# Optimization experiments

Measured on AMD Instinct MI355X. Metric: run time of the kernel, lower is better.

## Reference

```python
import jax, jax.numpy as jnp
import numpy as np

C = 256        # channels
H = 8          # num_heads
DH = C // H    # head dim
WIN = 512      # window size
STRIDE = 256
HID = 512      # ffn hidden = 2.0 * C
LENGTHS = [6400, 6400, 6400, 6400]
N = sum(LENGTHS)
EPS = 1e-5


def _build_windows(lengths, W, stride):
    # mirrors build_windows_1d: overlapping windows per segment, padded + masked
    idxs, masks = [], []
    start = 0
    for L in lengths:
        n_windows = max(0, L - 1) // stride + 1
        for i in range(n_windows):
            s = i * stride
            b = min(L, s + W)
            l = b - s
            loc = np.arange(s, b, dtype=np.int32) + start
            if l < W:
                loc = np.concatenate([loc, np.full(W - l, loc[-1], dtype=np.int32)])
            m = np.zeros(W, dtype=bool)
            m[:l] = True
            idxs.append(loc)
            masks.append(m)
        start += L
    return np.stack(idxs, 0), np.stack(masks, 0)


def _layernorm(x, w, b):
    mu = jnp.mean(x, axis=-1, keepdims=True)
    var = jnp.mean(jnp.square(x - mu), axis=-1, keepdims=True)
    return (x - mu) * jax.lax.rsqrt(var + EPS) * w + b


def setup_inputs() -> dict:
    key = jax.random.key(0)
    ks = jax.random.split(key, 8)
    win_idx_np, win_mask_np = _build_windows(LENGTHS, WIN, STRIDE)
    p = lambda k, shape: jax.random.normal(k, shape, dtype=jnp.float32) * 0.02
    return {
        "x": jax.random.normal(ks[0], (N, C), dtype=jnp.float32),
        "win_idx": jnp.asarray(win_idx_np, dtype=jnp.int32),
        "win_mask": jnp.asarray(win_mask_np),
        "ln1_w": jnp.ones((C,), jnp.float32),
        "ln1_b": jnp.zeros((C,), jnp.float32),
        "w_qkv": p(ks[1], (3 * C, C)),
        "w_proj": p(ks[2], (C, C)),
        "b_proj": jnp.zeros((C,), jnp.float32),
        "ln2_w": jnp.ones((C,), jnp.float32),
        "ln2_b": jnp.zeros((C,), jnp.float32),
        "w1": p(ks[3], (HID, C)),
        "b1": jnp.zeros((HID,), jnp.float32),
        "bn_w": jnp.ones((HID,), jnp.float32),
        "bn_b": jnp.zeros((HID,), jnp.float32),
        "w2": p(ks[4], (C, HID)),
        "b2": jnp.zeros((C,), jnp.float32),
    }


def reference(x, win_idx, win_mask, ln1_w, ln1_b, w_qkv, w_proj, b_proj,
              ln2_w, ln2_b, w1, b1, bn_w, bn_b, w2, b2):
    M, W = win_idx.shape
    x_in = _layernorm(x, ln1_w, ln1_b)                      # [N, C]
    g = x_in[win_idx]                                        # [M, W, C] gather
    qkv = (g @ w_qkv.T).reshape(M, W, 3, H, DH)
    qkv = jnp.moveaxis(qkv, (2, 3), (0, 2))                  # [3, M, H, W, DH]
    q, k, v = qkv[0], qkv[1], qkv[2]
    scores = jnp.einsum("mhqd,mhkd->mhqk", q, k) / jnp.sqrt(jnp.asarray(DH, x.dtype))
    scores = jnp.where(win_mask[:, None, None, :], scores, -jnp.inf)
    attn = jax.nn.softmax(scores, axis=-1)                   # [M, H, W, W]
    out = jnp.einsum("mhqk,mhkd->mhqd", attn, v)            # [M, H, W, DH]
    out = jnp.moveaxis(out, 1, 2).reshape(M, W, C)
    out_proj = (out @ w_proj.T + b_proj) * win_mask[..., None]
    flat_idx = win_idx.reshape(-1)
    y = jnp.zeros_like(x).at[flat_idx].add(out_proj.reshape(-1, C))
    counts = jnp.zeros((x.shape[0], 1), x.dtype).at[flat_idx].add(
        win_mask.reshape(-1, 1).astype(x.dtype))
    x1 = x + y / jnp.maximum(counts, 1.0)
    # FFN with training-mode BatchNorm1d (default norm_layer)
    h = _layernorm(x1, ln2_w, ln2_b) @ w1.T + b1             # [N, HID]
    mu = jnp.mean(h, axis=0)
    var = jnp.mean(jnp.square(h - mu), axis=0)
    h = (h - mu) * jax.lax.rsqrt(var + EPS) * bn_w + bn_b
    h = jax.nn.relu(h)
    return x1 + (h @ w2.T + b2)
```

## Files before the change

### kernel.cpp

```cpp
#include <hip/hip_runtime.h>

#define C_DIM 256
#define HID_DIM 512
#define NHEAD 8
#define DHEAD 32
#define WWIN 512

typedef __attribute__((ext_vector_type(8))) short frag_ab;
typedef __attribute__((ext_vector_type(4))) short frag4;
typedef __attribute__((ext_vector_type(4))) float f32x4;

__device__ __forceinline__ float bf2f(unsigned int u16) {
    return __uint_as_float(u16 << 16);
}
__device__ __forceinline__ unsigned short f2bf(float f) {
    unsigned int x = __float_as_uint(f);
    return (unsigned short)((x + 0x7fffu + ((x >> 16) & 1u)) >> 16);
}
__device__ __forceinline__ void unpack8(uint4 u, float* d) {
    d[0] = bf2f(u.x & 0xffffu); d[1] = bf2f(u.x >> 16);
    d[2] = bf2f(u.y & 0xffffu); d[3] = bf2f(u.y >> 16);
    d[4] = bf2f(u.z & 0xffffu); d[5] = bf2f(u.z >> 16);
    d[6] = bf2f(u.w & 0xffffu); d[7] = bf2f(u.w >> 16);
}
__device__ __forceinline__ unsigned int pk2(float lo, float hi) {
    return __builtin_amdgcn_perm(__float_as_uint(hi), __float_as_uint(lo), 0x07060302u);
}
__device__ __forceinline__ void async_cp16(const void* g, void* l) {
    __builtin_amdgcn_global_load_lds(
        (const __attribute__((address_space(1))) unsigned int*)g,
        (__attribute__((address_space(3))) unsigned int*)l, 16, 0, 0);
}

__global__ __launch_bounds__(256) void rowstats_k(const float* __restrict__ X,
        float* __restrict__ mu, float* __restrict__ rs) {
    int lane = threadIdx.x & 63;
    int row = blockIdx.x * 4 + (threadIdx.x >> 6);
    float4 v = ((const float4*)(X + (size_t)row * C_DIM))[lane];
    float s = v.x + v.y + v.z + v.w;
    float q = v.x * v.x + v.y * v.y + v.z * v.z + v.w * v.w;
    #pragma unroll
    for (int o = 32; o; o >>= 1) { s += __shfl_xor(s, o); q += __shfl_xor(q, o); }
    if (lane == 0) {
        float m = s * (1.0f / C_DIM);
        float var = q * (1.0f / C_DIM) - m * m;
        mu[row] = m; rs[row] = rsqrtf(var + 1e-5f);
    }
}

__global__ __launch_bounds__(512) void wininv_k(const int* __restrict__ widx,
        int* __restrict__ wlen, int* __restrict__ cnt, int* __restrict__ inv) {
    int m = blockIdx.x, j = threadIdx.x;
    int id = widx[m * WWIN + j];
    int valid = (j == 0) || (id != widx[m * WWIN + j - 1]);
    __shared__ int part[8];
    int v = valid;
    #pragma unroll
    for (int o = 32; o; o >>= 1) v += __shfl_xor(v, o);
    if ((j & 63) == 0) part[j >> 6] = v;
    __syncthreads();
    if (j == 0) {
        int s = 0;
        #pragma unroll
        for (int i = 0; i < 8; i++) s += part[i];
        wlen[m] = s;
    }
    if (valid) {
        int slot = atomicAdd(&cnt[id], 1);
        if (slot < 2) inv[id * 2 + slot] = m * WWIN + j;
    }
}

__global__ __launch_bounds__(256) void cvtw_k(
        const float* __restrict__ a, const float* __restrict__ b,
        const float* __restrict__ c, const float* __restrict__ d,
        unsigned short* __restrict__ oa, unsigned short* __restrict__ ob,
        unsigned short* __restrict__ oc, unsigned short* __restrict__ od) {
    int bi = blockIdx.x;
    const float* src; unsigned short* dst; int base;
    if (bi < 192)      { src = a; dst = oa; base = bi; }
    else if (bi < 256) { src = b; dst = ob; base = bi - 192; }
    else if (bi < 384) { src = c; dst = oc; base = bi - 256; }
    else               { src = d; dst = od; base = bi - 384; }
    int i = base * 1024 + threadIdx.x * 4;
    float4 v = *(const float4*)(src + i);
    ushort4 o;
    o.x = f2bf(v.x); o.y = f2bf(v.y); o.z = f2bf(v.z); o.w = f2bf(v.w);
    *(ushort4*)(dst + i) = o;
}

template<int K, int AMODE, int OMODE>
__global__ __launch_bounds__(256, 3) void mgemm_k(
        const void* __restrict__ Av, const unsigned short* __restrict__ Bw,
        const float* __restrict__ bias, void* __restrict__ Outv,
        const float* __restrict__ rowmu, const float* __restrict__ rowrs,
        const float* __restrict__ colw, const float* __restrict__ colb,
        const float* __restrict__ resid, float* __restrict__ hsum,
        float* __restrict__ hsq, int CN, int AM) {
    __shared__ unsigned short As[4096];
    __shared__ unsigned short Bs[4096];
    const int t = threadIdx.x;
    const int w = t >> 6, lane = t & 63;
    const int Q = lane >> 4, n = lane & 15;
    const int r0 = blockIdx.y * 128, c0 = blockIdx.x * 128;
    const int qr0 = (w & 1) * 64, qc0 = (w >> 1) * 64;
    const f32x4 z4 = {0.f, 0.f, 0.f, 0.f};
    f32x4 acc[4][4];
    #pragma unroll
    for (int i = 0; i < 4; i++)
        #pragma unroll
        for (int j = 0; j < 4; j++) acc[i][j] = z4;

    for (int k0 = 0; k0 < K; k0 += 32) {
        if (k0) __syncthreads();
        #pragma unroll
        for (int i = 0; i < 2; i++) {
            int sbase = w * 128 + i * 64;
            int l = sbase + lane;
            int col = l >> 2;
            int sub = ((l & 3) - (col >> 1)) & 3;
            async_cp16(Bw + (size_t)(c0 + col) * K + k0 + sub * 8, &Bs[sbase * 8]);
        }
        if constexpr (AMODE == 0 || AMODE == 4) {
            #pragma unroll
            for (int i = 0; i < 2; i++) {
                int sbase = w * 128 + i * 64;
                int l = sbase + lane;
                int row = l >> 2;
                int sub = ((l & 3) - (row >> 1)) & 3;
                const unsigned short* src;
                if constexpr (AMODE == 0)
                    src = (const unsigned short*)Av + (size_t)(r0 + row) * K + k0 + sub * 8;
                else
                    src = (const unsigned short*)Av + (size_t)k0 * AM + (size_t)(r0 + row) * 32 + sub * 8;
                async_cp16(src, &As[sbase * 8]);
            }
        } else {
            #pragma unroll
            for (int ii = 0; ii < 2; ii++) {
                int s = t + ii * 256;
                int row = s >> 2;
                int sub = ((s & 3) - (row >> 1)) & 3;
                const float* src = (const float*)Av + (size_t)(r0 + row) * K + k0 + sub * 8;
                float4 v0 = ((const float4*)src)[0];
                float4 v1 = ((const float4*)src)[1];
                float f[8] = {v0.x, v0.y, v0.z, v0.w, v1.x, v1.y, v1.z, v1.w};
                float4 cw0 = *(const float4*)(colw + k0 + sub * 8);
                float4 cw1 = *(const float4*)(colw + k0 + sub * 8 + 4);
                float4 cb0 = *(const float4*)(colb + k0 + sub * 8);
                float4 cb1 = *(const float4*)(colb + k0 + sub * 8 + 4);
                float cw[8] = {cw0.x, cw0.y, cw0.z, cw0.w, cw1.x, cw1.y, cw1.z, cw1.w};
                float cb[8] = {cb0.x, cb0.y, cb0.z, cb0.w, cb1.x, cb1.y, cb1.z, cb1.w};
                if constexpr (AMODE == 1) {
                    float rm = rowmu[r0 + row], rv = rowrs[r0 + row];
                    #pragma unroll
                    for (int j = 0; j < 8; j++) f[j] = (f[j] - rm) * rv * cw[j] + cb[j];
                } else {
                    #pragma unroll
                    for (int j = 0; j < 8; j++) f[j] = fmaxf(f[j] * cw[j] + cb[j], 0.f);
                }
                uint4 pkd;
                pkd.x = pk2(f[0], f[1]); pkd.y = pk2(f[2], f[3]);
                pkd.z = pk2(f[4], f[5]); pkd.w = pk2(f[6], f[7]);
                *(uint4*)&As[s * 8] = pkd;
            }
        }
        asm volatile("s_waitcnt vmcnt(0)" ::: "memory");
        __syncthreads();
        const int asub = (Q + (n >> 1)) & 3;
        frag_ab af[4], bfr[4];
        #pragma unroll
        for (int i = 0; i < 4; i++) {
            af[i]  = *(const frag_ab*)&As[((qr0 + i * 16 + n) * 4 + asub) * 8];
            bfr[i] = *(const frag_ab*)&Bs[((qc0 + i * 16 + n) * 4 + asub) * 8];
        }
        #pragma unroll
        for (int rt = 0; rt < 4; rt++)
            #pragma unroll
            for (int ct = 0; ct < 4; ct++)
                acc[rt][ct] = __builtin_amdgcn_mfma_f32_16x16x32_bf16(
                    af[rt], bfr[ct], acc[rt][ct], 0, 0, 0);
    }

    if constexpr (OMODE == 5) {
        __shared__ unsigned short Ts[4][16 * 72];
        unsigned short* tb = Ts[w];
        #pragma unroll
        for (int rt = 0; rt < 4; rt++) {
            #pragma unroll
            for (int ct = 0; ct < 4; ct++) {
                f32x4 a = acc[rt][ct];
                #pragma unroll
                for (int i = 0; i < 4; i++)
                    tb[(Q * 4 + i) * 72 + ct * 16 + n] = f2bf(a[i]);
            }
            int r2 = lane >> 2, sg = lane & 3;
            uint4 v0 = *(const uint4*)&tb[r2 * 72 + sg * 16];
            uint4 v1 = *(const uint4*)&tb[r2 * 72 + sg * 16 + 8];
            int mrow = r0 + qr0 + rt * 16 + r2;
            int ccb = c0 + qc0 + sg * 16;
            int plane = ((ccb >> 8) << 3) | ((ccb >> 5) & 7);
            unsigned short* dst = (unsigned short*)Outv +
                ((size_t)plane * CN + mrow) * 32 + (ccb & 31);
            *(uint4*)dst = v0;
            *(uint4*)(dst + 8) = v1;
        }
        return;
    }
    float sc[4] = {0.f, 0.f, 0.f, 0.f}, qc[4] = {0.f, 0.f, 0.f, 0.f};
    #pragma unroll
    for (int rt = 0; rt < 4; rt++) {
        #pragma unroll
        for (int ct = 0; ct < 4; ct++) {
            int mrow = r0 + qr0 + rt * 16 + Q * 4;
            int ccol = c0 + qc0 + ct * 16 + n;
            f32x4 a = acc[rt][ct];
            if constexpr (OMODE == 0) {
                unsigned short* dst = (unsigned short*)Outv + (size_t)mrow * CN + ccol;
                #pragma unroll
                for (int i = 0; i < 4; i++) dst[(size_t)i * CN] = f2bf(a[i]);
            } else if constexpr (OMODE == 1) {
                float bb = bias[ccol];
                unsigned short* dst = (unsigned short*)Outv + (size_t)mrow * CN + ccol;
                #pragma unroll
                for (int i = 0; i < 4; i++) dst[(size_t)i * CN] = f2bf(a[i] + bb);
            } else if constexpr (OMODE == 2) {
                float bb = bias[ccol];
                float* dst = (float*)Outv + (size_t)mrow * CN + ccol;
                #pragma unroll
                for (int i = 0; i < 4; i++) dst[(size_t)i * CN] = a[i] + bb;
            } else if constexpr (OMODE == 3) {
                float bb = bias[ccol];
                float* dst = (float*)Outv + (size_t)mrow * CN + ccol;
                #pragma unroll
                for (int i = 0; i < 4; i++) {
                    float v = a[i] + bb;
                    dst[(size_t)i * CN] = v;
                    sc[ct] += v; qc[ct] += v * v;
                }
            } else {
                float bb = bias[ccol];
                float* dst = (float*)Outv + (size_t)mrow * CN + ccol;
                const float* rr = resid + (size_t)mrow * CN + ccol;
                #pragma unroll
                for (int i = 0; i < 4; i++) dst[(size_t)i * CN] = a[i] + bb + rr[(size_t)i * CN];
            }
        }
    }
    if constexpr (OMODE == 3) {
        #pragma unroll
        for (int ct = 0; ct < 4; ct++) {
            float s = sc[ct], q2 = qc[ct];
            s += __shfl_xor(s, 16); s += __shfl_xor(s, 32);
            q2 += __shfl_xor(q2, 16); q2 += __shfl_xor(q2, 32);
            if (Q == 0) {
                int ccol = c0 + qc0 + ct * 16 + n;
                atomicAdd(&hsum[ccol], s);
                atomicAdd(&hsq[ccol], q2);
            }
        }
    }
}

#define KSTR 40
#define VSTR 136
#define TSTR 40
__global__ __launch_bounds__(256, 4) void attn_mfma_k(
        const unsigned short* __restrict__ qkv, const int* __restrict__ widx,
        const int* __restrict__ wlen, unsigned short* __restrict__ aout,
        int N, int MW) {
    __shared__ unsigned short Kl[128 * KSTR];
    __shared__ unsigned short Vt[32 * VSTR];
    __shared__ unsigned short Ts[4][16 * TSTR];
    const int mh = blockIdx.x >> 1, half = blockIdx.x & 1;
    const int m = mh >> 3, h = mh & 7;
    const int len = wlen[m];
    if (half && len <= 256) return;
    const int t = threadIdx.x;
    const int w = t >> 6, lane = t & 63;
    const int Q = lane >> 4, n = lane & 15;
    const int qbase = half * 256 + w * 64;
    const int* wrow = widx + m * WWIN;
    const unsigned short* Qp = qkv + (size_t)h * N * 32;
    const unsigned short* Kp = qkv + (size_t)(8 + h) * N * 32;
    const unsigned short* Vp = qkv + (size_t)(16 + h) * N * 32;
    const f32x4 z4 = {0.f, 0.f, 0.f, 0.f};

    const float qs = 0.17677669529663687f * 1.4426950408889634f;
    frag_ab qf[4];
    #pragma unroll
    for (int qt = 0; qt < 4; qt++) {
        int tok = wrow[qbase + qt * 16 + n];
        uint4 u = *(const uint4*)(Qp + (size_t)tok * 32 + Q * 8);
        float f[8]; unpack8(u, f);
        uint4 r;
        r.x = pk2(f[0] * qs, f[1] * qs); r.y = pk2(f[2] * qs, f[3] * qs);
        r.z = pk2(f[4] * qs, f[5] * qs); r.w = pk2(f[6] * qs, f[7] * qs);
        qf[qt] = __builtin_bit_cast(frag_ab, r);
    }

    f32x4 Ot[2][4];
    #pragma unroll
    for (int dt = 0; dt < 2; dt++)
        #pragma unroll
        for (int qt = 0; qt < 4; qt++) Ot[dt][qt] = z4;
    float rsum[4] = {0.f, 0.f, 0.f, 0.f};

    const int nchunk = (len + 127) >> 7;
    for (int c = 0; c < nchunk; c++) {
        const int kb = c << 7;
        __syncthreads();
        if (t < 128) {
            int r = t;
            int tok = wrow[kb + r];
            const uint4* src = (const uint4*)(Vp + (size_t)tok * 32);
            #pragma unroll
            for (int i = 0; i < 4; i++) {
                uint4 u = src[i];
                unsigned short* vp = &Vt[(i * 8) * VSTR + r];
                vp[0 * VSTR] = (unsigned short)(u.x & 0xffffu);
                vp[1 * VSTR] = (unsigned short)(u.x >> 16);
                vp[2 * VSTR] = (unsigned short)(u.y & 0xffffu);
                vp[3 * VSTR] = (unsigned short)(u.y >> 16);
                vp[4 * VSTR] = (unsigned short)(u.z & 0xffffu);
                vp[5 * VSTR] = (unsigned short)(u.z >> 16);
                vp[6 * VSTR] = (unsigned short)(u.w & 0xffffu);
                vp[7 * VSTR] = (unsigned short)(u.w >> 16);
            }
        } else {
            int r = t - 128;
            int tok = wrow[kb + r];
            const uint4* src = (const uint4*)(Kp + (size_t)tok * 32);
            #pragma unroll
            for (int i = 0; i < 4; i++) {
                int c4 = (r + i) & 3;
                *(uint4*)&Kl[r * KSTR + c4 * 8] = src[c4];
            }
        }
        __syncthreads();
        int rem = len - kb; if (rem > 128) rem = 128;
        const int nsub = (rem + 31) >> 5;
        for (int s = 0; s < nsub; s++) {
            const int lim = rem - s * 32;
            frag_ab kf0 = *(const frag_ab*)&Kl[(s * 32 + n) * KSTR + Q * 8];
            frag_ab kf1 = *(const frag_ab*)&Kl[(s * 32 + 16 + n) * KSTR + Q * 8];
            frag4 va00 = *(const frag4*)&Vt[n * VSTR + s * 32 + 4 * Q];
            frag4 va01 = *(const frag4*)&Vt[n * VSTR + s * 32 + 16 + 4 * Q];
            frag4 va10 = *(const frag4*)&Vt[(16 + n) * VSTR + s * 32 + 4 * Q];
            frag4 va11 = *(const frag4*)&Vt[(16 + n) * VSTR + s * 32 + 16 + 4 * Q];
            #pragma unroll
            for (int qt = 0; qt < 4; qt++) {
                f32x4 s0 = __builtin_amdgcn_mfma_f32_16x16x32_bf16(kf0, qf[qt], z4, 0, 0, 0);
                f32x4 s1 = __builtin_amdgcn_mfma_f32_16x16x32_bf16(kf1, qf[qt], z4, 0, 0, 0);
                float e[8];
                #pragma unroll
                for (int i = 0; i < 4; i++) {
                    e[i]     = __builtin_amdgcn_exp2f(s0[i]);
                    e[4 + i] = __builtin_amdgcn_exp2f(s1[i]);
                }
                if (lim < 32) {
                    #pragma unroll
                    for (int i = 0; i < 4; i++) {
                        if (4 * Q + i >= lim)      e[i] = 0.f;
                        if (16 + 4 * Q + i >= lim) e[4 + i] = 0.f;
                    }
                }
                float rsq = rsum[qt];
                #pragma unroll
                for (int i = 0; i < 8; i++) rsq += e[i];
                rsum[qt] = rsq;
                uint2 u0, u1;
                u0.x = pk2(e[0], e[1]); u0.y = pk2(e[2], e[3]);
                u1.x = pk2(e[4], e[5]); u1.y = pk2(e[6], e[7]);
                frag4 p0 = __builtin_bit_cast(frag4, u0);
                frag4 p1 = __builtin_bit_cast(frag4, u1);
                Ot[0][qt] = __builtin_amdgcn_mfma_f32_16x16x16bf16_1k(va00, p0, Ot[0][qt], 0, 0, 0);
                Ot[0][qt] = __builtin_amdgcn_mfma_f32_16x16x16bf16_1k(va01, p1, Ot[0][qt], 0, 0, 0);
                Ot[1][qt] = __builtin_amdgcn_mfma_f32_16x16x16bf16_1k(va10, p0, Ot[1][qt], 0, 0, 0);
                Ot[1][qt] = __builtin_amdgcn_mfma_f32_16x16x16bf16_1k(va11, p1, Ot[1][qt], 0, 0, 0);
            }
        }
    }

    unsigned short* tb = Ts[w];
    const int r2 = lane >> 2, sg = lane & 3;
    #pragma unroll
    for (int qt = 0; qt < 4; qt++) {
        float r = rsum[qt];
        r += __shfl_xor(r, 16);
        r += __shfl_xor(r, 32);
        float inv = 1.f / r;
        #pragma unroll
        for (int dt = 0; dt < 2; dt++) {
            f32x4 o = Ot[dt][qt];
            uint2 pk;
            pk.x = pk2(o[0] * inv, o[1] * inv);
            pk.y = pk2(o[2] * inv, o[3] * inv);
            *(uint2*)&tb[n * TSTR + dt * 16 + 4 * Q] = pk;
        }
        uint4 v = *(const uint4*)&tb[r2 * TSTR + sg * 8];
        unsigned short* dst = aout +
            ((size_t)h * MW + (size_t)(m * WWIN + qbase + qt * 16 + r2)) * 32 + sg * 8;
        *(uint4*)dst = v;
    }
}

__global__ __launch_bounds__(256) void combine_k(
        const float* __restrict__ x, const unsigned short* __restrict__ proj,
        const int* __restrict__ cnt, const int* __restrict__ inv,
        float* __restrict__ x1, float* __restrict__ mu, float* __restrict__ rs) {
    int lane = threadIdx.x & 63;
    int row = blockIdx.x * 4 + (threadIdx.x >> 6);
    int c = cnt[row];
    if (c > 2) c = 2;
    float4 acc = make_float4(0.f, 0.f, 0.f, 0.f);
    for (int s = 0; s < c; s++) {
        int src = inv[row * 2 + s];
        uint2 p = ((const uint2*)(proj + (size_t)src * C_DIM))[lane];
        acc.x += bf2f(p.x & 0xffffu); acc.y += bf2f(p.x >> 16);
        acc.z += bf2f(p.y & 0xffffu); acc.w += bf2f(p.y >> 16);
    }
    float ic = 1.f / (float)(c > 0 ? c : 1);
    float4 xv = ((const float4*)(x + (size_t)row * C_DIM))[lane];
    float4 r4;
    r4.x = xv.x + acc.x * ic; r4.y = xv.y + acc.y * ic;
    r4.z = xv.z + acc.z * ic; r4.w = xv.w + acc.w * ic;
    ((float4*)(x1 + (size_t)row * C_DIM))[lane] = r4;
    float s = r4.x + r4.y + r4.z + r4.w;
    float q = r4.x * r4.x + r4.y * r4.y + r4.z * r4.z + r4.w * r4.w;
    #pragma unroll
    for (int o = 32; o; o >>= 1) { s += __shfl_xor(s, o); q += __shfl_xor(q, o); }
    if (lane == 0) {
        float mm = s * (1.f / C_DIM);
        float var = q * (1.f / C_DIM) - mm * mm;
        mu[row] = mm; rs[row] = rsqrtf(var + 1e-5f);
    }
}

__global__ void bnfin_k(const float* __restrict__ hsum, const float* __restrict__ hsq,
        const float* __restrict__ bnw, const float* __restrict__ bnb,
        float* __restrict__ premul, float* __restrict__ preadd, float inv_n) {
    int c = threadIdx.x;
    float m = hsum[c] * inv_n;
    float var = hsq[c] * inv_n - m * m;
    float rstd = rsqrtf(var + 1e-5f);
    float pm = rstd * bnw[c];
    premul[c] = pm;
    preadd[c] = bnb[c] - m * pm;
}

extern "C" void kernel_launch(void* const* d_in, const int* in_sizes, int n_in,
                              void* d_out, int out_size, void* d_ws, size_t ws_size,
                              hipStream_t stream) {
    const float* x    = (const float*)d_in[0];
    const int* widx   = (const int*)d_in[1];
    const float* ln1w = (const float*)d_in[3];
    const float* ln1b = (const float*)d_in[4];
    const float* wqkv = (const float*)d_in[5];
    const float* wproj = (const float*)d_in[6];
    const float* bproj = (const float*)d_in[7];
    const float* ln2w = (const float*)d_in[8];
    const float* ln2b = (const float*)d_in[9];
    const float* w1   = (const float*)d_in[10];
    const float* b1   = (const float*)d_in[11];
    const float* bnw  = (const float*)d_in[12];
    const float* bnb  = (const float*)d_in[13];
    const float* w2   = (const float*)d_in[14];
    const float* b2   = (const float*)d_in[15];
    float* out = (float*)d_out;

    const int N  = in_sizes[0] / C_DIM;
    const int MW = in_sizes[1];
    const int M  = MW / WWIN;

    char* w = (char*)d_ws;
    size_t off = 0;
    auto alloc = [&](size_t bytes) -> void* {
        void* p = w + off;
        off += (bytes + 255) & ~(size_t)255;
        return p;
    };
    size_t szA = (size_t)MW * C_DIM * 4;
    void* regA = alloc(szA);
    unsigned short* qkv = (unsigned short*)regA;
    unsigned short* out_proj = (unsigned short*)regA;
    float* hbuf = (float*)regA;
    size_t szB = (size_t)MW * C_DIM * 2;
    void* regB = alloc(szB);
    unsigned short* attn_out = (unsigned short*)regB;
    float* x1 = (float*)regB;

    unsigned short* wqkv_bf = (unsigned short*)alloc(768 * 256 * 2);
    unsigned short* wproj_bf = (unsigned short*)alloc(256 * 256 * 2);
    unsigned short* w1_bf = (unsigned short*)alloc(512 * 256 * 2);
    unsigned short* w2_bf = (unsigned short*)alloc(256 * 512 * 2);

    float* mu0 = (float*)alloc((size_t)N * 4);
    float* rs0 = (float*)alloc((size_t)N * 4);
    float* mu1 = (float*)alloc((size_t)N * 4);
    float* rs1 = (float*)alloc((size_t)N * 4);
    int* cnt   = (int*)alloc((size_t)N * 4);
    int* inv   = (int*)alloc((size_t)N * 8);
    int* wlen  = (int*)alloc((size_t)M * 4);
    float* hsum = (float*)alloc(HID_DIM * 4);
    float* hsq  = (float*)alloc(HID_DIM * 4);
    float* premul = (float*)alloc(HID_DIM * 4);
    float* preadd = (float*)alloc(HID_DIM * 4);

    hipMemsetAsync(cnt, 0, (size_t)N * 4, stream);
    hipMemsetAsync(hsum, 0, HID_DIM * 4, stream);
    hipMemsetAsync(hsq, 0, HID_DIM * 4, stream);

    cvtw_k<<<512, 256, 0, stream>>>(wqkv, wproj, w1, w2, wqkv_bf, wproj_bf, w1_bf, w2_bf);
    rowstats_k<<<N / 4, 256, 0, stream>>>(x, mu0, rs0);
    wininv_k<<<M, 512, 0, stream>>>(widx, wlen, cnt, inv);
    mgemm_k<256, 1, 5><<<dim3(768 / 128, N / 128), 256, 0, stream>>>(
        x, wqkv_bf, nullptr, qkv, mu0, rs0, ln1w, ln1b, nullptr, nullptr, nullptr, N, 0);
    attn_mfma_k<<<M * NHEAD * 2, 256, 0, stream>>>(qkv, widx, wlen, attn_out, N, MW);
    mgemm_k<256, 4, 1><<<dim3(256 / 128, MW / 128), 256, 0, stream>>>(
        attn_out, wproj_bf, bproj, out_proj, nullptr, nullptr, nullptr, nullptr,
        nullptr, nullptr, nullptr, 256, MW);
    combine_k<<<N / 4, 256, 0, stream>>>(x, out_proj, cnt, inv, x1, mu1, rs1);
    mgemm_k<256, 1, 3><<<dim3(512 / 128, N / 128), 256, 0, stream>>>(
        x1, w1_bf, b1, hbuf, mu1, rs1, ln2w, ln2b, nullptr, hsum, hsq, 512, 0);
    bnfin_k<<<1, HID_DIM, 0, stream>>>(hsum, hsq, bnw, bnb, premul, preadd, 1.0f / (float)N);
    mgemm_k<512, 3, 4><<<dim3(256 / 128, N / 128), 256, 0, stream>>>(
        hbuf, w2_bf, b2, out, nullptr, nullptr, premul, preadd, x1, nullptr, nullptr, 256, 0);
}
```

Before: 300.3 us.

## Precompute LayerNorm outputs as bf16 and store GEMM intermediates in bf16

LayerNorm1 and LayerNorm2 are now applied in the row-stats and combine kernels, which write normalized bf16 activations. The QKV and FFN1 GEMMs can then load A tiles with async global-to-LDS copies instead of fp32 loads plus in-register normalization. The FFN hidden buffer and out_proj now go through an LDS-transposed bf16 epilogue with coalesced 16-byte stores, and the FFN2 A loader reads bf16 rather than fp32. This trades extra bf16 activation writes and reads for halved intermediate traffic and simpler GEMM prologues, at some precision cost because BN statistics are taken before bf16 rounding.

```diff
diff --git a/kernel.cpp b/kernel.cpp
--- a/kernel.cpp
+++ b/kernel.cpp
@@ -32,8 +32,9 @@
         (__attribute__((address_space(3))) unsigned int*)l, 16, 0, 0);
 }
 
-__global__ __launch_bounds__(256) void rowstats_k(const float* __restrict__ X,
-        float* __restrict__ mu, float* __restrict__ rs) {
+__global__ __launch_bounds__(256) void ln1_k(const float* __restrict__ X,
+        const float* __restrict__ wv, const float* __restrict__ bv,
+        unsigned short* __restrict__ out) {
     int lane = threadIdx.x & 63;
     int row = blockIdx.x * 4 + (threadIdx.x >> 6);
     float4 v = ((const float4*)(X + (size_t)row * C_DIM))[lane];
@@ -41,11 +42,14 @@
     float q = v.x * v.x + v.y * v.y + v.z * v.z + v.w * v.w;
     #pragma unroll
     for (int o = 32; o; o >>= 1) { s += __shfl_xor(s, o); q += __shfl_xor(q, o); }
-    if (lane == 0) {
-        float m = s * (1.0f / C_DIM);
-        float var = q * (1.0f / C_DIM) - m * m;
-        mu[row] = m; rs[row] = rsqrtf(var + 1e-5f);
-    }
+    float mm = s * (1.f / C_DIM);
+    float rv = rsqrtf(q * (1.f / C_DIM) - mm * mm + 1e-5f);
+    float4 w4 = ((const float4*)wv)[lane];
+    float4 b4 = ((const float4*)bv)[lane];
+    uint2 o2;
+    o2.x = pk2((v.x - mm) * rv * w4.x + b4.x, (v.y - mm) * rv * w4.y + b4.y);
+    o2.y = pk2((v.z - mm) * rv * w4.z + b4.z, (v.w - mm) * rv * w4.w + b4.w);
+    ((uint2*)(out + (size_t)row * C_DIM))[lane] = o2;
 }
 
 __global__ __launch_bounds__(512) void wininv_k(const int* __restrict__ widx,
@@ -93,7 +97,6 @@
 __global__ __launch_bounds__(256, 3) void mgemm_k(
         const void* __restrict__ Av, const unsigned short* __restrict__ Bw,
         const float* __restrict__ bias, void* __restrict__ Outv,
-        const float* __restrict__ rowmu, const float* __restrict__ rowrs,
         const float* __restrict__ colw, const float* __restrict__ colb,
         const float* __restrict__ resid, float* __restrict__ hsum,
         float* __restrict__ hsq, int CN, int AM) {
@@ -141,24 +144,17 @@
                 int s = t + ii * 256;
                 int row = s >> 2;
                 int sub = ((s & 3) - (row >> 1)) & 3;
-                const float* src = (const float*)Av + (size_t)(r0 + row) * K + k0 + sub * 8;
-                float4 v0 = ((const float4*)src)[0];
-                float4 v1 = ((const float4*)src)[1];
-                float f[8] = {v0.x, v0.y, v0.z, v0.w, v1.x, v1.y, v1.z, v1.w};
+                uint4 u = *(const uint4*)((const unsigned short*)Av +
+                        (size_t)(r0 + row) * K + k0 + sub * 8);
+                float f[8]; unpack8(u, f);
                 float4 cw0 = *(const float4*)(colw + k0 + sub * 8);
                 float4 cw1 = *(const float4*)(colw + k0 + sub * 8 + 4);
                 float4 cb0 = *(const float4*)(colb + k0 + sub * 8);
                 float4 cb1 = *(const float4*)(colb + k0 + sub * 8 + 4);
                 float cw[8] = {cw0.x, cw0.y, cw0.z, cw0.w, cw1.x, cw1.y, cw1.z, cw1.w};
                 float cb[8] = {cb0.x, cb0.y, cb0.z, cb0.w, cb1.x, cb1.y, cb1.z, cb1.w};
-                if constexpr (AMODE == 1) {
-                    float rm = rowmu[r0 + row], rv = rowrs[r0 + row];
-                    #pragma unroll
-                    for (int j = 0; j < 8; j++) f[j] = (f[j] - rm) * rv * cw[j] + cb[j];
-                } else {
-                    #pragma unroll
-                    for (int j = 0; j < 8; j++) f[j] = fmaxf(f[j] * cw[j] + cb[j], 0.f);
-                }
+                #pragma unroll
+                for (int j = 0; j < 8; j++) f[j] = fmaxf(f[j] * cw[j] + cb[j], 0.f);
                 uint4 pkd;
                 pkd.x = pk2(f[0], f[1]); pkd.y = pk2(f[2], f[3]);
                 pkd.z = pk2(f[4], f[5]); pkd.w = pk2(f[6], f[7]);
@@ -182,32 +178,57 @@
                     af[rt], bfr[ct], acc[rt][ct], 0, 0, 0);
     }
 
-    if constexpr (OMODE == 5) {
+    if constexpr (OMODE == 5 || OMODE == 6 || OMODE == 7) {
         __shared__ unsigned short Ts[4][16 * 72];
         unsigned short* tb = Ts[w];
+        float sc[4] = {0.f, 0.f, 0.f, 0.f}, qc[4] = {0.f, 0.f, 0.f, 0.f};
+        const int r2 = lane >> 2, sg = lane & 3;
         #pragma unroll
         for (int rt = 0; rt < 4; rt++) {
             #pragma unroll
             for (int ct = 0; ct < 4; ct++) {
+                float bb = 0.f;
+                if constexpr (OMODE != 5) bb = bias[c0 + qc0 + ct * 16 + n];
                 f32x4 a = acc[rt][ct];
                 #pragma unroll
-                for (int i = 0; i < 4; i++)
-                    tb[(Q * 4 + i) * 72 + ct * 16 + n] = f2bf(a[i]);
-            }
-            int r2 = lane >> 2, sg = lane & 3;
+                for (int i = 0; i < 4; i++) {
+                    float v = a[i] + bb;
+                    if constexpr (OMODE == 6) { sc[ct] += v; qc[ct] += v * v; }
+                    tb[(Q * 4 + i) * 72 + ct * 16 + n] = f2bf(v);
+                }
+            }
             uint4 v0 = *(const uint4*)&tb[r2 * 72 + sg * 16];
             uint4 v1 = *(const uint4*)&tb[r2 * 72 + sg * 16 + 8];
             int mrow = r0 + qr0 + rt * 16 + r2;
-            int ccb = c0 + qc0 + sg * 16;
-            int plane = ((ccb >> 8) << 3) | ((ccb >> 5) & 7);
-            unsigned short* dst = (unsigned short*)Outv +
-                ((size_t)plane * CN + mrow) * 32 + (ccb & 31);
-            *(uint4*)dst = v0;
-            *(uint4*)(dst + 8) = v1;
+            if constexpr (OMODE == 5) {
+                int ccb = c0 + qc0 + sg * 16;
+                int plane = ((ccb >> 8) << 3) | ((ccb >> 5) & 7);
+                unsigned short* dst = (unsigned short*)Outv +
+                    ((size_t)plane * CN + mrow) * 32 + (ccb & 31);
+                *(uint4*)dst = v0;
+                *(uint4*)(dst + 8) = v1;
+            } else {
+                unsigned short* dst = (unsigned short*)Outv +
+                    (size_t)mrow * CN + c0 + qc0 + sg * 16;
+                *(uint4*)dst = v0;
+                *(uint4*)(dst + 8) = v1;
+            }
+        }
+        if constexpr (OMODE == 6) {
+            #pragma unroll
+            for (int ct = 0; ct < 4; ct++) {
+                float s = sc[ct], q2 = qc[ct];
+                s += __shfl_xor(s, 16); s += __shfl_xor(s, 32);
+                q2 += __shfl_xor(q2, 16); q2 += __shfl_xor(q2, 32);
+                if (Q == 0) {
+                    int ccol = c0 + qc0 + ct * 16 + n;
+                    atomicAdd(&hsum[ccol], s);
+                    atomicAdd(&hsq[ccol], q2);
+                }
+            }
         }
         return;
     }
-    float sc[4] = {0.f, 0.f, 0.f, 0.f}, qc[4] = {0.f, 0.f, 0.f, 0.f};
     #pragma unroll
     for (int rt = 0; rt < 4; rt++) {
         #pragma unroll
@@ -215,49 +236,11 @@
             int mrow = r0 + qr0 + rt * 16 + Q * 4;
             int ccol = c0 + qc0 + ct * 16 + n;
             f32x4 a = acc[rt][ct];
-            if constexpr (OMODE == 0) {
-                unsigned short* dst = (unsigned short*)Outv + (size_t)mrow * CN + ccol;
-                #pragma unroll
-                for (int i = 0; i < 4; i++) dst[(size_t)i * CN] = f2bf(a[i]);
-            } else if constexpr (OMODE == 1) {
-                float bb = bias[ccol];
-                unsigned short* dst = (unsigned short*)Outv + (size_t)mrow * CN + ccol;
-                #pragma unroll
-                for (int i = 0; i < 4; i++) dst[(size_t)i * CN] = f2bf(a[i] + bb);
-            } else if constexpr (OMODE == 2) {
-                float bb = bias[ccol];
-                float* dst = (float*)Outv + (size_t)mrow * CN + ccol;
-                #pragma unroll
-                for (int i = 0; i < 4; i++) dst[(size_t)i * CN] = a[i] + bb;
-            } else if constexpr (OMODE == 3) {
-                float bb = bias[ccol];
-                float* dst = (float*)Outv + (size_t)mrow * CN + ccol;
-                #pragma unroll
-                for (int i = 0; i < 4; i++) {
-                    float v = a[i] + bb;
-                    dst[(size_t)i * CN] = v;
-                    sc[ct] += v; qc[ct] += v * v;
-                }
-            } else {
-                float bb = bias[ccol];
-                float* dst = (float*)Outv + (size_t)mrow * CN + ccol;
-                const float* rr = resid + (size_t)mrow * CN + ccol;
-                #pragma unroll
-                for (int i = 0; i < 4; i++) dst[(size_t)i * CN] = a[i] + bb + rr[(size_t)i * CN];
-            }
-        }
-    }
-    if constexpr (OMODE == 3) {
-        #pragma unroll
-        for (int ct = 0; ct < 4; ct++) {
-            float s = sc[ct], q2 = qc[ct];
-            s += __shfl_xor(s, 16); s += __shfl_xor(s, 32);
-            q2 += __shfl_xor(q2, 16); q2 += __shfl_xor(q2, 32);
-            if (Q == 0) {
-                int ccol = c0 + qc0 + ct * 16 + n;
-                atomicAdd(&hsum[ccol], s);
-                atomicAdd(&hsq[ccol], q2);
-            }
+            float bb = bias[ccol];
+            float* dst = (float*)Outv + (size_t)mrow * CN + ccol;
+            const float* rr = resid + (size_t)mrow * CN + ccol;
+            #pragma unroll
+            for (int i = 0; i < 4; i++) dst[(size_t)i * CN] = a[i] + bb + rr[(size_t)i * CN];
         }
     }
 }
@@ -408,7 +391,8 @@
 __global__ __launch_bounds__(256) void combine_k(
         const float* __restrict__ x, const unsigned short* __restrict__ proj,
         const int* __restrict__ cnt, const int* __restrict__ inv,
-        float* __restrict__ x1, float* __restrict__ mu, float* __restrict__ rs) {
+        float* __restrict__ x1, unsigned short* __restrict__ x1ln,
+        const float* __restrict__ ln2w, const float* __restrict__ ln2b) {
     int lane = threadIdx.x & 63;
     int row = blockIdx.x * 4 + (threadIdx.x >> 6);
     int c = cnt[row];
@@ -430,11 +414,14 @@
     float q = r4.x * r4.x + r4.y * r4.y + r4.z * r4.z + r4.w * r4.w;
     #pragma unroll
     for (int o = 32; o; o >>= 1) { s += __shfl_xor(s, o); q += __shfl_xor(q, o); }
-    if (lane == 0) {
-        float mm = s * (1.f / C_DIM);
-        float var = q * (1.f / C_DIM) - mm * mm;
-        mu[row] = mm; rs[row] = rsqrtf(var + 1e-5f);
-    }
+    float mm = s * (1.f / C_DIM);
+    float rv = rsqrtf(q * (1.f / C_DIM) - mm * mm + 1e-5f);
+    float4 w4 = ((const float4*)ln2w)[lane];
+    float4 b4 = ((const float4*)ln2b)[lane];
+    uint2 o2;
+    o2.x = pk2((r4.x - mm) * rv * w4.x + b4.x, (r4.y - mm) * rv * w4.y + b4.y);
+    o2.y = pk2((r4.z - mm) * rv * w4.z + b4.z, (r4.w - mm) * rv * w4.w + b4.w);
+    ((uint2*)(x1ln + (size_t)row * C_DIM))[lane] = o2;
 }
 
 __global__ void bnfin_k(const float* __restrict__ hsum, const float* __restrict__ hsq,
@@ -481,10 +468,12 @@
         return p;
     };
     size_t szA = (size_t)MW * C_DIM * 4;
-    void* regA = alloc(szA);
+    char* regA = (char*)alloc(szA);
     unsigned short* qkv = (unsigned short*)regA;
+    unsigned short* x_ln = (unsigned short*)(regA + (size_t)1536 * N);
     unsigned short* out_proj = (unsigned short*)regA;
-    float* hbuf = (float*)regA;
+    unsigned short* x1ln = (unsigned short*)(regA + (size_t)1024 * N);
+    unsigned short* hbuf = (unsigned short*)regA;
     size_t szB = (size_t)MW * C_DIM * 2;
     void* regB = alloc(szB);
     unsigned short* attn_out = (unsigned short*)regB;
@@ -495,10 +484,6 @@
     unsigned short* w1_bf = (unsigned short*)alloc(512 * 256 * 2);
     unsigned short* w2_bf = (unsigned short*)alloc(256 * 512 * 2);
 
-    float* mu0 = (float*)alloc((size_t)N * 4);
-    float* rs0 = (float*)alloc((size_t)N * 4);
-    float* mu1 = (float*)alloc((size_t)N * 4);
-    float* rs1 = (float*)alloc((size_t)N * 4);
     int* cnt   = (int*)alloc((size_t)N * 4);
     int* inv   = (int*)alloc((size_t)N * 8);
     int* wlen  = (int*)alloc((size_t)M * 4);
@@ -512,18 +497,18 @@
     hipMemsetAsync(hsq, 0, HID_DIM * 4, stream);
 
     cvtw_k<<<512, 256, 0, stream>>>(wqkv, wproj, w1, w2, wqkv_bf, wproj_bf, w1_bf, w2_bf);
-    rowstats_k<<<N / 4, 256, 0, stream>>>(x, mu0, rs0);
+    ln1_k<<<N / 4, 256, 0, stream>>>(x, ln1w, ln1b, x_ln);
     wininv_k<<<M, 512, 0, stream>>>(widx, wlen, cnt, inv);
-    mgemm_k<256, 1, 5><<<dim3(768 / 128, N / 128), 256, 0, stream>>>(
-        x, wqkv_bf, nullptr, qkv, mu0, rs0, ln1w, ln1b, nullptr, nullptr, nullptr, N, 0);
+    mgemm_k<256, 0, 5><<<dim3(768 / 128, N / 128), 256, 0, stream>>>(
+        x_ln, wqkv_bf, nullptr, qkv, nullptr, nullptr, nullptr, nullptr, nullptr, N, 0);
     attn_mfma_k<<<M * NHEAD * 2, 256, 0, stream>>>(qkv, widx, wlen, attn_out, N, MW);
-    mgemm_k<256, 4, 1><<<dim3(256 / 128, MW / 128), 256, 0, stream>>>(
-        attn_out, wproj_bf, bproj, out_proj, nullptr, nullptr, nullptr, nullptr,
-        nullptr, nullptr, nullptr, 256, MW);
-    combine_k<<<N / 4, 256, 0, stream>>>(x, out_proj, cnt, inv, x1, mu1, rs1);
-    mgemm_k<256, 1, 3><<<dim3(512 / 128, N / 128), 256, 0, stream>>>(
-        x1, w1_bf, b1, hbuf, mu1, rs1, ln2w, ln2b, nullptr, hsum, hsq, 512, 0);
+    mgemm_k<256, 4, 7><<<dim3(256 / 128, MW / 128), 256, 0, stream>>>(
+        attn_out, wproj_bf, bproj, out_proj, nullptr, nullptr, nullptr,
+        nullptr, nullptr, 256, MW);
+    combine_k<<<N / 4, 256, 0, stream>>>(x, out_proj, cnt, inv, x1, x1ln, ln2w, ln2b);
+    mgemm_k<256, 0, 6><<<dim3(512 / 128, N / 128), 256, 0, stream>>>(
+        x1ln, w1_bf, b1, hbuf, nullptr, nullptr, nullptr, hsum, hsq, 512, 0);
     bnfin_k<<<1, HID_DIM, 0, stream>>>(hsum, hsq, bnw, bnb, premul, preadd, 1.0f / (float)N);
-    mgemm_k<512, 3, 4><<<dim3(256 / 128, N / 128), 256, 0, stream>>>(
-        hbuf, w2_bf, b2, out, nullptr, nullptr, premul, preadd, x1, nullptr, nullptr, 256, 0);
-}
+    mgemm_k<512, 2, 4><<<dim3(256 / 128, N / 128), 256, 0, stream>>>(
+        hbuf, w2_bf, b2, out, premul, preadd, x1, nullptr, nullptr, 256, 0);
+}
```

New measurement: 273.7 us. -8.9%, faster.
